# Performance work log

Hardware: AMD Instinct MI355X
Metric: run time of the kernel (lower is better)

The kernel has to match this reference:

```python
import jax, jax.numpy as jnp
import numpy as np
from jax import lax

B, T, H, E, V, S = 32, 512, 1024, 300, 32000, 50
NL2 = 4  # 2 layers * 2 directions of encoder hidden


def setup_inputs() -> dict:
    key = jax.random.key(0)
    ks = jax.random.split(key, 20)
    w = 0.05  # small init scale to keep tanh/softmax well-conditioned
    return {
        "enc_out": jax.random.normal(ks[0], (B, T, H), jnp.float32),
        "enc_h": jax.random.normal(ks[1], (NL2, B, H // 2), jnp.float32),
        "enc_c": jax.random.normal(ks[2], (NL2, B, H // 2), jnp.float32),
        "embedding": jax.random.normal(ks[3], (V, E), jnp.float32),
        "attn_W": jax.random.normal(ks[4], (H, 2 * H), jnp.float32) * w,
        "attn_b": jnp.zeros((H,), jnp.float32),
        "v": jax.random.normal(ks[5], (H,), jnp.float32) * w,
        "Wih0": jax.random.normal(ks[6], (4 * H, E + H), jnp.float32) * w,
        "Whh0": jax.random.normal(ks[7], (4 * H, H), jnp.float32) * w,
        "bih0": jnp.zeros((4 * H,), jnp.float32),
        "bhh0": jnp.zeros((4 * H,), jnp.float32),
        "Wih1": jax.random.normal(ks[8], (4 * H, H), jnp.float32) * w,
        "Whh1": jax.random.normal(ks[9], (4 * H, H), jnp.float32) * w,
        "bih1": jnp.zeros((4 * H,), jnp.float32),
        "bhh1": jnp.zeros((4 * H,), jnp.float32),
        "genW": jax.random.normal(ks[10], (V, H), jnp.float32) * w,
        "genb": jnp.zeros((V,), jnp.float32),
        "question": jax.random.randint(ks[11], (B, S), 0, V, jnp.int64),
    }


def _lstm_cell(x, h, c, Wih, Whh, bih, bhh):
    # torch gate order: i, f, g, o
    g = x @ Wih.T + bih + h @ Whh.T + bhh
    i, f, gg, o = jnp.split(g, 4, axis=-1)
    c2 = jax.nn.sigmoid(f) * c + jax.nn.sigmoid(i) * jnp.tanh(gg)
    h2 = jax.nn.sigmoid(o) * jnp.tanh(c2)
    return h2, c2


def reference(enc_out, enc_h, enc_c, embedding, attn_W, attn_b, v,
              Wih0, Whh0, bih0, bhh0, Wih1, Whh1, bih1, bhh1,
              genW, genb, question):
    # merge bidirectional encoder halves: (2L,B,H/2) -> (L,B,H)
    h0 = jnp.concatenate([enc_h[0::2], enc_h[1::2]], axis=2)
    c0 = jnp.concatenate([enc_c[0::2], enc_c[1::2]], axis=2)

    def step(carry, tok):
        h, c = carry  # each (L, B, H)
        emb = embedding[tok]  # (B, E); dropout is identity (eval mode)
        hid = h[-1]  # (B, H), last-layer hidden drives attention
        Hrep = jnp.broadcast_to(hid[:, None, :], enc_out.shape)  # (B,T,H)
        energy = jnp.tanh(jnp.concatenate([Hrep, enc_out], axis=-1) @ attn_W.T + attn_b)
        scores = jnp.einsum('bth,h->bt', energy, v)
        aw = jax.nn.softmax(scores, axis=1)  # (B, T)
        ctx = jnp.einsum('bt,bth->bh', aw, enc_out)  # (B, H)
        x = jnp.concatenate([emb, ctx], axis=-1)  # (B, E+H)
        h0n, c0n = _lstm_cell(x, h[0], c[0], Wih0, Whh0, bih0, bhh0)
        h1n, c1n = _lstm_cell(h0n, h[1], c[1], Wih1, Whh1, bih1, bhh1)
        out = jax.nn.log_softmax(h1n @ genW.T + genb, axis=-1)  # (B, V)
        return (jnp.stack([h0n, h1n]), jnp.stack([c0n, c1n])), out

    _, outs = lax.scan(step, (h0, c0), question.T)  # outs: (S, B, V)
    return jnp.transpose(outs, (1, 0, 2))  # (B, S, V)
```

## Files before the change

### kernel.cpp

```cpp
#include <hip/hip_runtime.h>
#include <hip/hip_bf16.h>
#include <math.h>

#define DEVI static __device__ __forceinline__

namespace {
constexpr int B = 32, T = 512, H = 1024, E = 300, V = 32000, S = 50;
constexpr int KX = E + H;
constexpr int K0 = 2368;
constexpr int K1 = 2048;
constexpr int MG = V + H;
}

typedef __bf16 bf16x8 __attribute__((ext_vector_type(8)));
typedef float f32x4 __attribute__((ext_vector_type(4)));

DEVI float bf2f(unsigned short u) { union { unsigned int i; float f; } v; v.i = (unsigned int)u << 16; return v.f; }
DEVI unsigned short f2bf(float f) {
  union { float f; unsigned int i; } v; v.f = f;
  unsigned int x = v.i;
  return (unsigned short)((x + 0x7fffu + ((x >> 16) & 1u)) >> 16);
}
#if __has_builtin(__builtin_amdgcn_rcpf)
DEVI float frcp(float x) { return __builtin_amdgcn_rcpf(x); }
#else
DEVI float frcp(float x) { return 1.0f / x; }
#endif
DEVI float sigm(float x) { return frcp(1.0f + __expf(-x)); }
DEVI float tanh_(float x) { return 1.0f - 2.0f * frcp(__expf(2.0f * x) + 1.0f); }

__global__ __launch_bounds__(256) void k_cast_gen(const float* __restrict__ genW,
    const float* __restrict__ attn_W, unsigned short* __restrict__ Wbig) {
  size_t i4 = ((size_t)blockIdx.x * 256 + threadIdx.x) * 4;
  if (i4 >= (size_t)MG * H) return;
  int row = (int)(i4 >> 10), k = (int)(i4 & 1023);
  const float* src = row < V ? &genW[((size_t)row << 10) + k]
                             : &attn_W[(size_t)(row - V) * (2 * H) + k];
  float4 v = *(const float4*)src;
  ushort4 o; o.x = f2bf(v.x); o.y = f2bf(v.y); o.z = f2bf(v.z); o.w = f2bf(v.w);
  *(ushort4*)&Wbig[i4] = o;
}

__global__ __launch_bounds__(256) void k_cast_l0(const float* __restrict__ Wih,
    const float* __restrict__ Whh, unsigned short* __restrict__ Wc) {
  int m = blockIdx.x;
  int g = m & 3, n = m >> 2, srow = g * H + n;
  for (int i = threadIdx.x; i < K0 / 4; i += 256) {
    int k = i * 4;
    float4 v;
    if (k < KX) v = *(const float4*)&Wih[(size_t)srow * KX + k];
    else if (k < KX + H) v = *(const float4*)&Whh[(size_t)srow * H + (k - KX)];
    else v = make_float4(0.f, 0.f, 0.f, 0.f);
    ushort4 o; o.x = f2bf(v.x); o.y = f2bf(v.y); o.z = f2bf(v.z); o.w = f2bf(v.w);
    *(ushort4*)&Wc[(size_t)m * K0 + k] = o;
  }
}

__global__ __launch_bounds__(256) void k_cast_l1(const float* __restrict__ Wih,
    const float* __restrict__ Whh, unsigned short* __restrict__ Wc) {
  int m = blockIdx.x;
  int g = m & 3, n = m >> 2, srow = g * H + n;
  for (int i = threadIdx.x; i < K1 / 4; i += 256) {
    int k = i * 4;
    float4 v = (k < H) ? *(const float4*)&Wih[(size_t)srow * H + k]
                       : *(const float4*)&Whh[(size_t)srow * H + (k - H)];
    ushort4 o; o.x = f2bf(v.x); o.y = f2bf(v.y); o.z = f2bf(v.z); o.w = f2bf(v.w);
    *(ushort4*)&Wc[(size_t)m * K1 + k] = o;
  }
}

__global__ __launch_bounds__(256) void k_cast_attnr(const float* __restrict__ attn_W,
                                                    unsigned short* __restrict__ Wr) {
  size_t i4 = ((size_t)blockIdx.x * 256 + threadIdx.x) * 4;
  if (i4 >= (size_t)H * H) return;
  int n = (int)(i4 >> 10), k = (int)(i4 & 1023);
  float4 v = *(const float4*)&attn_W[(size_t)n * (2 * H) + H + k];
  ushort4 o; o.x = f2bf(v.x); o.y = f2bf(v.y); o.z = f2bf(v.z); o.w = f2bf(v.w);
  *(ushort4*)&Wr[i4] = o;
}

__global__ void k_bias(const float* bih0, const float* bhh0,
                       const float* bih1, const float* bhh1,
                       float* bc0, float* bc1) {
  int idx = blockIdx.x * 256 + threadIdx.x;
  if (idx < 4096) { int g = idx & 3, n = idx >> 2; bc0[idx] = bih0[g * H + n] + bhh0[g * H + n]; }
  else if (idx < 8192) { int m = idx - 4096; int g = m & 3, n = m >> 2; bc1[m] = bih1[g * H + n] + bhh1[g * H + n]; }
}

__global__ __launch_bounds__(256) void k_cast_enc(const float* __restrict__ src,
                                                  unsigned short* __restrict__ dst) {
  size_t i4 = ((size_t)blockIdx.x * 256 + threadIdx.x) * 4;
  if (i4 >= (size_t)B * T * H) return;
  float4 v = *(const float4*)&src[i4];
  ushort4 o; o.x = f2bf(v.x); o.y = f2bf(v.y); o.z = f2bf(v.z); o.w = f2bf(v.w);
  *(ushort4*)&dst[i4] = o;
}

__global__ __launch_bounds__(256) void k_init(const float* __restrict__ enc_h,
    const float* __restrict__ enc_c, float* __restrict__ cbuf,
    unsigned short* __restrict__ xc0_0, unsigned short* __restrict__ xc0_1,
    unsigned short* __restrict__ xc1_0, unsigned short* __restrict__ hgen) {
  int idx = blockIdx.x * 256 + threadIdx.x;
  if (idx < 2 * B * H) {
    int l = idx >> 15, r = idx & 32767, b = r >> 10, hh = r & 1023;
    int half = hh >> 9, hr = hh & 511;
    int src = (2 * l + half) * B * (H / 2) + b * (H / 2) + hr;
    cbuf[idx] = enc_c[src];
    unsigned short hb = f2bf(enc_h[src]);
    if (l == 0) xc0_0[(size_t)b * K0 + KX + hh] = hb;
    else { xc1_0[(size_t)b * K1 + H + hh] = hb; hgen[(size_t)b * H + hh] = hb; }
  } else if (idx < 2 * B * H + 2 * B * 20) {
    int j = idx - 2 * B * H;
    int p = j / (B * 20), rr = j % (B * 20), b = rr / 20, kk = rr % 20;
    (p ? xc0_1 : xc0_0)[(size_t)b * K0 + KX + H + kk] = 0;
  }
}

__global__ __launch_bounds__(256) void k_encproj_mfma(const unsigned short* __restrict__ Wr,
    const unsigned short* __restrict__ Xb, const float* __restrict__ attn_b,
    unsigned short* __restrict__ encp) {
  int wv = threadIdx.x >> 6, lane = threadIdx.x & 63;
  int n0w = blockIdx.x * 64 + wv * 16;
  int m0 = blockIdx.y * 64;
  const unsigned short* Wp = Wr + (size_t)(n0w + (lane & 15)) * H + (lane >> 4) * 8;
  const unsigned short* Xp = Xb + (size_t)(m0 + (lane & 15)) * H + (lane >> 4) * 8;
  f32x4 acc[4] = {{0.f,0.f,0.f,0.f},{0.f,0.f,0.f,0.f},{0.f,0.f,0.f,0.f},{0.f,0.f,0.f,0.f}};
#pragma unroll 2
  for (int k0 = 0; k0 < H; k0 += 32) {
    bf16x8 a = *(const bf16x8*)(Wp + k0);
#pragma unroll
    for (int g = 0; g < 4; g++) {
      bf16x8 b = *(const bf16x8*)(Xp + (size_t)g * 16 * H + k0);
      acc[g] = __builtin_amdgcn_mfma_f32_16x16x32_bf16(a, b, acc[g], 0, 0, 0);
    }
  }
  int nb = n0w + (lane >> 4) * 4;
  f32x4 bi = *(const f32x4*)&attn_b[nb];
#pragma unroll
  for (int g = 0; g < 4; g++) {
    int m = m0 + g * 16 + (lane & 15);
    f32x4 o = acc[g] + bi;
    ushort4 ob; ob.x = f2bf(o[0]); ob.y = f2bf(o[1]); ob.z = f2bf(o[2]); ob.w = f2bf(o[3]);
    *(ushort4*)&encp[(size_t)m * H + nb] = ob;
  }
}

template <int K>
DEVI void gemm_tile(const unsigned short* __restrict__ W, const unsigned short* __restrict__ X,
                    int m0w, int lane, f32x4& acc0, f32x4& acc1) {
  const unsigned short* Wp = W + (size_t)(m0w + (lane & 15)) * K + (lane >> 4) * 8;
  const unsigned short* Xp = X + (size_t)(lane & 15) * K + (lane >> 4) * 8;
#pragma unroll 4
  for (int k0 = 0; k0 < K; k0 += 32) {
    bf16x8 a  = *(const bf16x8*)(Wp + k0);
    bf16x8 b0 = *(const bf16x8*)(Xp + k0);
    bf16x8 b1 = *(const bf16x8*)(Xp + 16 * K + k0);
    acc0 = __builtin_amdgcn_mfma_f32_16x16x32_bf16(a, b0, acc0, 0, 0, 0);
    acc1 = __builtin_amdgcn_mfma_f32_16x16x32_bf16(a, b1, acc1, 0, 0, 0);
  }
}

template <int K>
__global__ __launch_bounds__(256) void k_gemm_out(const unsigned short* __restrict__ W,
    const unsigned short* __restrict__ X, const float* __restrict__ bias, int M0,
    float* __restrict__ out0, int ld0, float* __restrict__ out1, int ld1,
    float* __restrict__ part) {
  __shared__ float esum[4][32];
  int wv = threadIdx.x >> 6, lane = threadIdx.x & 63;
  int m0w = blockIdx.x * 64 + wv * 16;
  f32x4 acc0 = {0.f, 0.f, 0.f, 0.f}, acc1 = acc0;
  gemm_tile<K>(W, X, m0w, lane, acc0, acc1);
  int r0 = m0w + (lane >> 4) * 4;
  int b = lane & 15;
  float s0 = 0.f, s1 = 0.f;
  if (r0 < M0) {
    f32x4 bi = *(const f32x4*)&bias[r0];
    f32x4 o0 = acc0 + bi, o1 = acc1 + bi;
    *(f32x4*)&out0[(size_t)b * ld0 + r0] = o0;
    *(f32x4*)&out0[(size_t)(b + 16) * ld0 + r0] = o1;
    s0 = __expf(o0[0]) + __expf(o0[1]) + __expf(o0[2]) + __expf(o0[3]);
    s1 = __expf(o1[0]) + __expf(o1[1]) + __expf(o1[2]) + __expf(o1[3]);
  } else {
    int r = r0 - M0;
    *(f32x4*)&out1[(size_t)b * ld1 + r] = acc0;
    *(f32x4*)&out1[(size_t)(b + 16) * ld1 + r] = acc1;
  }
  if (part != nullptr && blockIdx.x < V / 64) {
    s0 += __shfl_xor(s0, 16, 64); s0 += __shfl_xor(s0, 32, 64);
    s1 += __shfl_xor(s1, 16, 64); s1 += __shfl_xor(s1, 32, 64);
    if (lane < 16) { esum[wv][lane] = s0; esum[wv][lane + 16] = s1; }
    __syncthreads();
    if (threadIdx.x < 32)
      part[blockIdx.x * 32 + threadIdx.x] =
          esum[0][threadIdx.x] + esum[1][threadIdx.x] + esum[2][threadIdx.x] + esum[3][threadIdx.x];
  }
}

template <int K>
__global__ __launch_bounds__(256) void k_gemm_lstm(const unsigned short* __restrict__ W,
    const unsigned short* __restrict__ X, const float* __restrict__ bcomb,
    float* __restrict__ c,
    unsigned short* __restrict__ hA, int ldA_, int offA,
    unsigned short* __restrict__ hB, int ldB_, int offB) {
  __shared__ f32x4 red[4][64][2];
  int wv = threadIdx.x >> 6, lane = threadIdx.x & 63;
  int m0w = blockIdx.x * 16;
  const unsigned short* Wp = W + (size_t)(m0w + (lane & 15)) * K + (lane >> 4) * 8;
  const unsigned short* Xp = X + (size_t)(lane & 15) * K + (lane >> 4) * 8;
  f32x4 acc0 = {0.f, 0.f, 0.f, 0.f}, acc1 = acc0;
#pragma unroll 2
  for (int k0 = wv * 32; k0 < K; k0 += 128) {
    bf16x8 a  = *(const bf16x8*)(Wp + k0);
    bf16x8 b0 = *(const bf16x8*)(Xp + k0);
    bf16x8 b1 = *(const bf16x8*)(Xp + 16 * K + k0);
    acc0 = __builtin_amdgcn_mfma_f32_16x16x32_bf16(a, b0, acc0, 0, 0, 0);
    acc1 = __builtin_amdgcn_mfma_f32_16x16x32_bf16(a, b1, acc1, 0, 0, 0);
  }
  red[wv][lane][0] = acc0;
  red[wv][lane][1] = acc1;
  __syncthreads();
  if (wv == 0) {
    acc0 = red[0][lane][0] + red[1][lane][0] + red[2][lane][0] + red[3][lane][0];
    acc1 = red[0][lane][1] + red[1][lane][1] + red[2][lane][1] + red[3][lane][1];
    int r0 = m0w + (lane >> 4) * 4;
    int n = r0 >> 2;
    f32x4 bi = *(const f32x4*)&bcomb[r0];
#pragma unroll
    for (int f = 0; f < 2; f++) {
      f32x4 g = f ? acc1 : acc0;
      int b = (lane & 15) + f * 16;
      float gi = g[0] + bi[0], gf = g[1] + bi[1];
      float gg = g[2] + bi[2], go = g[3] + bi[3];
      float cp = c[(size_t)b * H + n];
      float c2 = sigm(gf) * cp + sigm(gi) * tanh_(gg);
      c[(size_t)b * H + n] = c2;
      unsigned short hb = f2bf(sigm(go) * tanh_(c2));
      hA[(size_t)b * ldA_ + offA + n] = hb;
      hB[(size_t)b * ldB_ + offB + n] = hb;
    }
  }
}

__global__ __launch_bounds__(256) void k_p1(const unsigned short* __restrict__ encp,
    const float* __restrict__ hidproj, const float* __restrict__ vvec,
    float* __restrict__ scores,
    const float* __restrict__ logits, const float* __restrict__ part,
    float* __restrict__ out,
    const float* __restrict__ embedding, const int* __restrict__ question,
    unsigned short* __restrict__ xc, int s) {
  int bx = blockIdx.x, tid = threadIdx.x;
  if (bx < 4096) {
    int wid = bx * 4 + (tid >> 6);
    int lane = tid & 63;
    int b = wid >> 9;
    const unsigned short* ep = encp + (size_t)wid * H;
    const float* hp = hidproj + (size_t)b * H;
    float acc = 0.f;
#pragma unroll
    for (int i = 0; i < 2; i++) {
      int base = i * 512 + lane * 8;
      uint4 u = *(const uint4*)&ep[base];
      float4 h0 = *(const float4*)&hp[base];
      float4 h1 = *(const float4*)&hp[base + 4];
      float4 v0 = *(const float4*)&vvec[base];
      float4 v1 = *(const float4*)&vvec[base + 4];
      acc += v0.x * tanh_(bf2f((unsigned short)(u.x & 0xffff)) + h0.x);
      acc += v0.y * tanh_(bf2f((unsigned short)(u.x >> 16)) + h0.y);
      acc += v0.z * tanh_(bf2f((unsigned short)(u.y & 0xffff)) + h0.z);
      acc += v0.w * tanh_(bf2f((unsigned short)(u.y >> 16)) + h0.w);
      acc += v1.x * tanh_(bf2f((unsigned short)(u.z & 0xffff)) + h1.x);
      acc += v1.y * tanh_(bf2f((unsigned short)(u.z >> 16)) + h1.y);
      acc += v1.z * tanh_(bf2f((unsigned short)(u.w & 0xffff)) + h1.z);
      acc += v1.w * tanh_(bf2f((unsigned short)(u.w >> 16)) + h1.w);
    }
#pragma unroll
    for (int off = 32; off; off >>= 1) acc += __shfl_xor(acc, off, 64);
    if (lane == 0) scores[wid] = acc;
  } else if (bx < 4352) {
    if (s == 0) return;
    __shared__ float red[256];
    int idx = bx - 4096;
    int b = idx >> 3, ch = idx & 7;
    float ssum = 0.f;
    for (int i = tid; i < V / 64; i += 256) ssum += part[i * 32 + b];
    red[tid] = ssum; __syncthreads();
    for (int st = 128; st; st >>= 1) { if (tid < st) red[tid] += red[tid + st]; __syncthreads(); }
    float lse = __logf(red[0]);
    const float* L = logits + (size_t)b * V + ch * 4000;
    float* O = out + ((size_t)b * S + (s - 1)) * V + ch * 4000;
    for (int i = tid; i < 1000; i += 256) {
      float4 v = ((const float4*)L)[i];
      ((float4*)O)[i] = make_float4(v.x - lse, v.y - lse, v.z - lse, v.w - lse);
    }
  } else {
    int b = bx - 4352;
    int tok = question[b * S + s];
    for (int e = tid; e < E; e += 256)
      xc[(size_t)b * K0 + e] = f2bf(embedding[(size_t)tok * E + e]);
  }
}

__global__ __launch_bounds__(256) void k_ctx(const float* __restrict__ scores,
    const unsigned short* __restrict__ enc_bf, unsigned short* __restrict__ xc) {
  int b = blockIdx.x, y = blockIdx.y, tid = threadIdx.x;
  __shared__ float aw[T];
  __shared__ float red[256];
  float s0 = scores[b * T + tid], s1 = scores[b * T + 256 + tid];
  float m = fmaxf(s0, s1);
  red[tid] = m; __syncthreads();
  for (int st = 128; st; st >>= 1) { if (tid < st) red[tid] = fmaxf(red[tid], red[tid + st]); __syncthreads(); }
  m = red[0]; __syncthreads();
  float e0 = __expf(s0 - m), e1 = __expf(s1 - m);
  aw[tid] = e0; aw[tid + 256] = e1;
  red[tid] = e0 + e1; __syncthreads();
  for (int st = 128; st; st >>= 1) { if (tid < st) red[tid] += red[tid + st]; __syncthreads(); }
  float inv = frcp(red[0]);
  __syncthreads();
  int wv = tid >> 6, l = tid & 63;
  int q = l & 15, tp = l >> 4;
  const unsigned short* eb = enc_bf + (size_t)b * T * H + y * 64 + q * 4;
  float a0 = 0.f, a1 = 0.f, a2 = 0.f, a3 = 0.f;
  for (int it = 0; it < 32; it++) {
    int t = it * 16 + wv * 4 + tp;
    uint2 u = *(const uint2*)&eb[(size_t)t * H];
    float w = aw[t];
    a0 += w * bf2f((unsigned short)(u.x & 0xffff));
    a1 += w * bf2f((unsigned short)(u.x >> 16));
    a2 += w * bf2f((unsigned short)(u.y & 0xffff));
    a3 += w * bf2f((unsigned short)(u.y >> 16));
  }
  a0 += __shfl_xor(a0, 16, 64); a0 += __shfl_xor(a0, 32, 64);
  a1 += __shfl_xor(a1, 16, 64); a1 += __shfl_xor(a1, 32, 64);
  a2 += __shfl_xor(a2, 16, 64); a2 += __shfl_xor(a2, 32, 64);
  a3 += __shfl_xor(a3, 16, 64); a3 += __shfl_xor(a3, 32, 64);
  __syncthreads();
  if (tp == 0) {
    red[wv * 64 + q * 4 + 0] = a0; red[wv * 64 + q * 4 + 1] = a1;
    red[wv * 64 + q * 4 + 2] = a2; red[wv * 64 + q * 4 + 3] = a3;
  }
  __syncthreads();
  if (tid < 64) {
    float val = (red[tid] + red[64 + tid] + red[128 + tid] + red[192 + tid]) * inv;
    xc[(size_t)b * K0 + E + y * 64 + tid] = f2bf(val);
  }
}

__global__ __launch_bounds__(256) void k_lsB(const float* __restrict__ logits,
    const float* __restrict__ part, float* __restrict__ out, int s) {
  int b = blockIdx.x, ch = blockIdx.y, tid = threadIdx.x;
  __shared__ float red[256];
  float ssum = 0.f;
  for (int i = tid; i < V / 64; i += 256) ssum += part[i * 32 + b];
  red[tid] = ssum; __syncthreads();
  for (int st = 128; st; st >>= 1) { if (tid < st) red[tid] += red[tid + st]; __syncthreads(); }
  float lse = __logf(red[0]);
  const float* L = logits + (size_t)b * V + ch * 4000;
  float* O = out + ((size_t)b * S + s) * V + ch * 4000;
  for (int i = tid; i < 1000; i += 256) {
    float4 v = ((const float4*)L)[i];
    ((float4*)O)[i] = make_float4(v.x - lse, v.y - lse, v.z - lse, v.w - lse);
  }
}

extern "C" void kernel_launch(void* const* d_in, const int* in_sizes, int n_in,
                              void* d_out, int out_size, void* d_ws, size_t ws_size,
                              hipStream_t stream) {
  const float* enc_out   = (const float*)d_in[0];
  const float* enc_h     = (const float*)d_in[1];
  const float* enc_c     = (const float*)d_in[2];
  const float* embedding = (const float*)d_in[3];
  const float* attn_W    = (const float*)d_in[4];
  const float* attn_b    = (const float*)d_in[5];
  const float* vvec      = (const float*)d_in[6];
  const float* Wih0      = (const float*)d_in[7];
  const float* Whh0      = (const float*)d_in[8];
  const float* bih0      = (const float*)d_in[9];
  const float* bhh0      = (const float*)d_in[10];
  const float* Wih1      = (const float*)d_in[11];
  const float* Whh1      = (const float*)d_in[12];
  const float* bih1      = (const float*)d_in[13];
  const float* bhh1      = (const float*)d_in[14];
  const float* genW      = (const float*)d_in[15];
  const float* genb      = (const float*)d_in[16];
  const int*   question  = (const int*)d_in[17];
  float* out = (float*)d_out;

  char* w = (char*)d_ws;
  auto alloc = [&](size_t bytes) { char* r = w; w += (bytes + 255) & ~(size_t)255; return r; };
  unsigned short* Wbig  = (unsigned short*)alloc((size_t)MG * H * 2);
  unsigned short* Wc0   = (unsigned short*)alloc((size_t)4096 * K0 * 2);
  unsigned short* Wc1   = (unsigned short*)alloc((size_t)4096 * K1 * 2);
  unsigned short* encb  = (unsigned short*)alloc((size_t)B * T * H * 2);
  unsigned short* encp  = (unsigned short*)alloc((size_t)B * T * H * 2);
  unsigned short* Wr    = (unsigned short*)alloc((size_t)H * H * 2);
  float* bcomb0 = (float*)alloc(4096 * 4);
  float* bcomb1 = (float*)alloc(4096 * 4);
  float* cbuf   = (float*)alloc((size_t)2 * B * H * 4);
  unsigned short* xc0[2] = {(unsigned short*)alloc((size_t)B * K0 * 2),
                            (unsigned short*)alloc((size_t)B * K0 * 2)};
  unsigned short* xc1[2] = {(unsigned short*)alloc((size_t)B * K1 * 2),
                            (unsigned short*)alloc((size_t)B * K1 * 2)};
  unsigned short* hgen  = (unsigned short*)alloc((size_t)B * H * 2);
  float* hidproj = (float*)alloc((size_t)B * H * 4);
  float* scores  = (float*)alloc((size_t)B * T * 4);
  float* logits  = (float*)alloc((size_t)B * V * 4);
  float* part    = (float*)alloc((size_t)(V / 64) * 32 * 4);

  k_cast_gen<<<(int)(((size_t)MG * H / 4 + 255) / 256), 256, 0, stream>>>(genW, attn_W, Wbig);
  k_cast_l0<<<4096, 256, 0, stream>>>(Wih0, Whh0, Wc0);
  k_cast_l1<<<4096, 256, 0, stream>>>(Wih1, Whh1, Wc1);
  k_cast_attnr<<<H * H / 4 / 256, 256, 0, stream>>>(attn_W, Wr);
  k_bias<<<32, 256, 0, stream>>>(bih0, bhh0, bih1, bhh1, bcomb0, bcomb1);
  k_cast_enc<<<(B * T * H / 4) / 256, 256, 0, stream>>>(enc_out, encb);
  k_init<<<(2 * B * H + 2 * B * 20 + 255) / 256, 256, 0, stream>>>(
      enc_h, enc_c, cbuf, xc0[0], xc0[1], xc1[0], hgen);
  k_encproj_mfma<<<dim3(H / 64, B * T / 64), 256, 0, stream>>>(Wr, encb, attn_b, encp);
  k_gemm_out<1024><<<H / 64, 256, 0, stream>>>(
      Wbig + (size_t)V * H, hgen, nullptr, 0, nullptr, 0, hidproj, H, nullptr);

  for (int s = 0; s < S; s++) {
    int par = s & 1;
    k_p1<<<4384, 256, 0, stream>>>(encp, hidproj, vvec, scores,
                                   logits, part, out, embedding, question, xc0[par], s);
    k_ctx<<<dim3(B, 16), 256, 0, stream>>>(scores, encb, xc0[par]);
    k_gemm_lstm<K0><<<4096 / 16, 256, 0, stream>>>(
        Wc0, xc0[par], bcomb0, cbuf,
        xc0[par ^ 1], K0, KX,
        xc1[par], K1, 0);
    k_gemm_lstm<K1><<<4096 / 16, 256, 0, stream>>>(
        Wc1, xc1[par], bcomb1, cbuf + B * H,
        xc1[par ^ 1], K1, H,
        hgen, H, 0);
    k_gemm_out<1024><<<MG / 64, 256, 0, stream>>>(
        Wbig, hgen, genb, V, logits, V, hidproj, H, part);
  }
  k_lsB<<<dim3(B, 8), 256, 0, stream>>>(logits, part, out, S - 1);
}
```

Baseline: 3.957 ms.

## Defer vocab projection GEMM into next step's attention kernel to shorten critical path

```diff
diff --git a/kernel.cpp b/kernel.cpp
--- a/kernel.cpp
+++ b/kernel.cpp
@@ -244,13 +244,37 @@
 __global__ __launch_bounds__(256) void k_p1(const unsigned short* __restrict__ encp,
     const float* __restrict__ hidproj, const float* __restrict__ vvec,
     float* __restrict__ scores,
-    const float* __restrict__ logits, const float* __restrict__ part,
+    const unsigned short* __restrict__ Wbig, const unsigned short* __restrict__ hgen,
+    const float* __restrict__ genb,
+    float* __restrict__ logitsW, float* __restrict__ partW,
+    const float* __restrict__ logitsR, const float* __restrict__ partR,
     float* __restrict__ out,
     const float* __restrict__ embedding, const int* __restrict__ question,
     unsigned short* __restrict__ xc, int s) {
   int bx = blockIdx.x, tid = threadIdx.x;
-  if (bx < 4096) {
-    int wid = bx * 4 + (tid >> 6);
+  if (bx < 500) {
+    if (s == 0) return;
+    __shared__ float esum[4][32];
+    int wv = tid >> 6, lane = tid & 63;
+    int m0w = bx * 64 + wv * 16;
+    f32x4 acc0 = {0.f, 0.f, 0.f, 0.f}, acc1 = acc0;
+    gemm_tile<1024>(Wbig, hgen, m0w, lane, acc0, acc1);
+    int r0 = m0w + (lane >> 4) * 4;
+    int b = lane & 15;
+    f32x4 bi = *(const f32x4*)&genb[r0];
+    f32x4 o0 = acc0 + bi, o1 = acc1 + bi;
+    *(f32x4*)&logitsW[(size_t)b * V + r0] = o0;
+    *(f32x4*)&logitsW[(size_t)(b + 16) * V + r0] = o1;
+    float s0 = __expf(o0[0]) + __expf(o0[1]) + __expf(o0[2]) + __expf(o0[3]);
+    float s1 = __expf(o1[0]) + __expf(o1[1]) + __expf(o1[2]) + __expf(o1[3]);
+    s0 += __shfl_xor(s0, 16, 64); s0 += __shfl_xor(s0, 32, 64);
+    s1 += __shfl_xor(s1, 16, 64); s1 += __shfl_xor(s1, 32, 64);
+    if (lane < 16) { esum[wv][lane] = s0; esum[wv][lane + 16] = s1; }
+    __syncthreads();
+    if (tid < 32)
+      partW[bx * 32 + tid] = esum[0][tid] + esum[1][tid] + esum[2][tid] + esum[3][tid];
+  } else if (bx < 4596) {
+    int wid = (bx - 500) * 4 + (tid >> 6);
     int lane = tid & 63;
     int b = wid >> 9;
     const unsigned short* ep = encp + (size_t)wid * H;
@@ -276,24 +300,24 @@
 #pragma unroll
     for (int off = 32; off; off >>= 1) acc += __shfl_xor(acc, off, 64);
     if (lane == 0) scores[wid] = acc;
-  } else if (bx < 4352) {
-    if (s == 0) return;
+  } else if (bx < 4852) {
+    if (s < 2) return;
     __shared__ float red[256];
-    int idx = bx - 4096;
+    int idx = bx - 4596;
     int b = idx >> 3, ch = idx & 7;
     float ssum = 0.f;
-    for (int i = tid; i < V / 64; i += 256) ssum += part[i * 32 + b];
+    for (int i = tid; i < V / 64; i += 256) ssum += partR[i * 32 + b];
     red[tid] = ssum; __syncthreads();
     for (int st = 128; st; st >>= 1) { if (tid < st) red[tid] += red[tid + st]; __syncthreads(); }
     float lse = __logf(red[0]);
-    const float* L = logits + (size_t)b * V + ch * 4000;
-    float* O = out + ((size_t)b * S + (s - 1)) * V + ch * 4000;
+    const float* L = logitsR + (size_t)b * V + ch * 4000;
+    float* O = out + ((size_t)b * S + (s - 2)) * V + ch * 4000;
     for (int i = tid; i < 1000; i += 256) {
       float4 v = ((const float4*)L)[i];
       ((float4*)O)[i] = make_float4(v.x - lse, v.y - lse, v.z - lse, v.w - lse);
     }
   } else {
-    int b = bx - 4352;
+    int b = bx - 4852;
     int tok = question[b * S + s];
     for (int e = tid; e < E; e += 256)
       xc[(size_t)b * K0 + e] = f2bf(embedding[(size_t)tok * E + e]);
@@ -403,8 +427,8 @@
   unsigned short* hgen  = (unsigned short*)alloc((size_t)B * H * 2);
   float* hidproj = (float*)alloc((size_t)B * H * 4);
   float* scores  = (float*)alloc((size_t)B * T * 4);
-  float* logits  = (float*)alloc((size_t)B * V * 4);
-  float* part    = (float*)alloc((size_t)(V / 64) * 32 * 4);
+  float* logits[2] = {(float*)alloc((size_t)B * V * 4), (float*)alloc((size_t)B * V * 4)};
+  float* part[2]   = {(float*)alloc((size_t)(V / 64) * 32 * 4), (float*)alloc((size_t)(V / 64) * 32 * 4)};
 
   k_cast_gen<<<(int)(((size_t)MG * H / 4 + 255) / 256), 256, 0, stream>>>(genW, attn_W, Wbig);
   k_cast_l0<<<4096, 256, 0, stream>>>(Wih0, Whh0, Wc0);
@@ -420,8 +444,11 @@
 
   for (int s = 0; s < S; s++) {
     int par = s & 1;
-    k_p1<<<4384, 256, 0, stream>>>(encp, hidproj, vvec, scores,
-                                   logits, part, out, embedding, question, xc0[par], s);
+    k_p1<<<4884, 256, 0, stream>>>(encp, hidproj, vvec, scores,
+                                   Wbig, hgen, genb,
+                                   logits[par ^ 1], part[par ^ 1],
+                                   logits[par], part[par],
+                                   out, embedding, question, xc0[par], s);
     k_ctx<<<dim3(B, 16), 256, 0, stream>>>(scores, encb, xc0[par]);
     k_gemm_lstm<K0><<<4096 / 16, 256, 0, stream>>>(
         Wc0, xc0[par], bcomb0, cbuf,
@@ -431,8 +458,11 @@
         Wc1, xc1[par], bcomb1, cbuf + B * H,
         xc1[par ^ 1], K1, H,
         hgen, H, 0);
-    k_gemm_out<1024><<<MG / 64, 256, 0, stream>>>(
-        Wbig, hgen, genb, V, logits, V, hidproj, H, part);
-  }
-  k_lsB<<<dim3(B, 8), 256, 0, stream>>>(logits, part, out, S - 1);
-}
+    k_gemm_out<1024><<<H / 64, 256, 0, stream>>>(
+        Wbig + (size_t)V * H, hgen, nullptr, 0, nullptr, 0, hidproj, H, nullptr);
+  }
+  k_gemm_out<1024><<<V / 64, 256, 0, stream>>>(
+      Wbig, hgen, genb, V, logits[(S - 1) & 1], V, hidproj, H, part[(S - 1) & 1]);
+  k_lsB<<<dim3(B, 8), 256, 0, stream>>>(logits[(S - 2) & 1], part[(S - 2) & 1], out, S - 2);
+  k_lsB<<<dim3(B, 8), 256, 0, stream>>>(logits[(S - 1) & 1], part[(S - 1) & 1], out, S - 1);
+}
```

Result: slower. 4.037 ms (+2.0%).

## Quantize generator and attention-hidden weights to FP8 and rebatch score kernel

Applied to the files above, without the earlier changes.

```diff
diff --git a/kernel.cpp b/kernel.cpp
--- a/kernel.cpp
+++ b/kernel.cpp
@@ -20,6 +20,23 @@
   union { float f; unsigned int i; } v; v.f = f;
   unsigned int x = v.i;
   return (unsigned short)((x + 0x7fffu + ((x >> 16) & 1u)) >> 16);
+}
+DEVI unsigned char f2e4m3(float x) {
+  union { float f; unsigned int u; } v;
+  v.f = x;
+  unsigned int s = (v.u >> 24) & 0x80u;
+  v.u &= 0x7FFFFFFFu;
+  if (v.f >= 448.0f) return (unsigned char)(s | 0x7E);
+  if (v.f < 0.015625f) {
+    int q = (int)rintf(v.f * 512.0f);
+    return (unsigned char)(s | (unsigned int)q);
+  }
+  unsigned int u = v.u;
+  unsigned int lsb = (u >> 20) & 1u;
+  u += 0x0007FFFFu + lsb;
+  unsigned int exp = (u >> 23) - 120u;
+  unsigned int man = (u >> 20) & 7u;
+  return (unsigned char)(s | (exp << 3) | man);
 }
 #if __has_builtin(__builtin_amdgcn_rcpf)
 DEVI float frcp(float x) { return __builtin_amdgcn_rcpf(x); }
@@ -30,15 +47,15 @@
 DEVI float tanh_(float x) { return 1.0f - 2.0f * frcp(__expf(2.0f * x) + 1.0f); }
 
 __global__ __launch_bounds__(256) void k_cast_gen(const float* __restrict__ genW,
-    const float* __restrict__ attn_W, unsigned short* __restrict__ Wbig) {
+    const float* __restrict__ attn_W, unsigned char* __restrict__ Wbig8) {
   size_t i4 = ((size_t)blockIdx.x * 256 + threadIdx.x) * 4;
   if (i4 >= (size_t)MG * H) return;
   int row = (int)(i4 >> 10), k = (int)(i4 & 1023);
   const float* src = row < V ? &genW[((size_t)row << 10) + k]
                              : &attn_W[(size_t)(row - V) * (2 * H) + k];
   float4 v = *(const float4*)src;
-  ushort4 o; o.x = f2bf(v.x); o.y = f2bf(v.y); o.z = f2bf(v.z); o.w = f2bf(v.w);
-  *(ushort4*)&Wbig[i4] = o;
+  uchar4 o; o.x = f2e4m3(v.x); o.y = f2e4m3(v.y); o.z = f2e4m3(v.z); o.w = f2e4m3(v.w);
+  *(uchar4*)&Wbig8[i4] = o;
 }
 
 __global__ __launch_bounds__(256) void k_cast_l0(const float* __restrict__ Wih,
@@ -99,16 +116,16 @@
 __global__ __launch_bounds__(256) void k_init(const float* __restrict__ enc_h,
     const float* __restrict__ enc_c, float* __restrict__ cbuf,
     unsigned short* __restrict__ xc0_0, unsigned short* __restrict__ xc0_1,
-    unsigned short* __restrict__ xc1_0, unsigned short* __restrict__ hgen) {
+    unsigned short* __restrict__ xc1_0, unsigned char* __restrict__ hgen8) {
   int idx = blockIdx.x * 256 + threadIdx.x;
   if (idx < 2 * B * H) {
     int l = idx >> 15, r = idx & 32767, b = r >> 10, hh = r & 1023;
     int half = hh >> 9, hr = hh & 511;
     int src = (2 * l + half) * B * (H / 2) + b * (H / 2) + hr;
     cbuf[idx] = enc_c[src];
-    unsigned short hb = f2bf(enc_h[src]);
-    if (l == 0) xc0_0[(size_t)b * K0 + KX + hh] = hb;
-    else { xc1_0[(size_t)b * K1 + H + hh] = hb; hgen[(size_t)b * H + hh] = hb; }
+    float hv = enc_h[src];
+    if (l == 0) xc0_0[(size_t)b * K0 + KX + hh] = f2bf(hv);
+    else { xc1_0[(size_t)b * K1 + H + hh] = f2bf(hv); hgen8[(size_t)b * H + hh] = f2e4m3(hv); }
   } else if (idx < 2 * B * H + 2 * B * 20) {
     int j = idx - 2 * B * H;
     int p = j / (B * 20), rr = j % (B * 20), b = rr / 20, kk = rr % 20;
@@ -145,31 +162,29 @@
   }
 }
 
-template <int K>
-DEVI void gemm_tile(const unsigned short* __restrict__ W, const unsigned short* __restrict__ X,
-                    int m0w, int lane, f32x4& acc0, f32x4& acc1) {
-  const unsigned short* Wp = W + (size_t)(m0w + (lane & 15)) * K + (lane >> 4) * 8;
-  const unsigned short* Xp = X + (size_t)(lane & 15) * K + (lane >> 4) * 8;
+DEVI void gemm_tile_fp8(const unsigned char* __restrict__ W, const unsigned char* __restrict__ X,
+                        int m0w, int lane, f32x4& acc0, f32x4& acc1) {
+  const unsigned char* Wp = W + (size_t)(m0w + (lane & 15)) * 1024 + (lane >> 4) * 8;
+  const unsigned char* Xp = X + (size_t)(lane & 15) * 1024 + (lane >> 4) * 8;
 #pragma unroll 4
-  for (int k0 = 0; k0 < K; k0 += 32) {
-    bf16x8 a  = *(const bf16x8*)(Wp + k0);
-    bf16x8 b0 = *(const bf16x8*)(Xp + k0);
-    bf16x8 b1 = *(const bf16x8*)(Xp + 16 * K + k0);
-    acc0 = __builtin_amdgcn_mfma_f32_16x16x32_bf16(a, b0, acc0, 0, 0, 0);
-    acc1 = __builtin_amdgcn_mfma_f32_16x16x32_bf16(a, b1, acc1, 0, 0, 0);
-  }
-}
-
-template <int K>
-__global__ __launch_bounds__(256) void k_gemm_out(const unsigned short* __restrict__ W,
-    const unsigned short* __restrict__ X, const float* __restrict__ bias, int M0,
+  for (int k0 = 0; k0 < 1024; k0 += 32) {
+    long a  = *(const long*)(Wp + k0);
+    long b0 = *(const long*)(Xp + k0);
+    long b1 = *(const long*)(Xp + 16 * 1024 + k0);
+    acc0 = __builtin_amdgcn_mfma_f32_16x16x32_fp8_fp8(a, b0, acc0, 0, 0, 0);
+    acc1 = __builtin_amdgcn_mfma_f32_16x16x32_fp8_fp8(a, b1, acc1, 0, 0, 0);
+  }
+}
+
+__global__ __launch_bounds__(256) void k_gemm_out_fp8(const unsigned char* __restrict__ W,
+    const unsigned char* __restrict__ X, const float* __restrict__ bias, int M0,
     float* __restrict__ out0, int ld0, float* __restrict__ out1, int ld1,
     float* __restrict__ part) {
   __shared__ float esum[4][32];
   int wv = threadIdx.x >> 6, lane = threadIdx.x & 63;
   int m0w = blockIdx.x * 64 + wv * 16;
   f32x4 acc0 = {0.f, 0.f, 0.f, 0.f}, acc1 = acc0;
-  gemm_tile<K>(W, X, m0w, lane, acc0, acc1);
+  gemm_tile_fp8(W, X, m0w, lane, acc0, acc1);
   int r0 = m0w + (lane >> 4) * 4;
   int b = lane & 15;
   float s0 = 0.f, s1 = 0.f;
@@ -201,7 +216,8 @@
     const unsigned short* __restrict__ X, const float* __restrict__ bcomb,
     float* __restrict__ c,
     unsigned short* __restrict__ hA, int ldA_, int offA,
-    unsigned short* __restrict__ hB, int ldB_, int offB) {
+    unsigned short* __restrict__ hB, int ldB_, int offB,
+    unsigned char* __restrict__ h8) {
   __shared__ f32x4 red[4][64][2];
   int wv = threadIdx.x >> 6, lane = threadIdx.x & 63;
   int m0w = blockIdx.x * 16;
@@ -234,9 +250,11 @@
       float cp = c[(size_t)b * H + n];
       float c2 = sigm(gf) * cp + sigm(gi) * tanh_(gg);
       c[(size_t)b * H + n] = c2;
-      unsigned short hb = f2bf(sigm(go) * tanh_(c2));
+      float h2 = sigm(go) * tanh_(c2);
+      unsigned short hb = f2bf(h2);
       hA[(size_t)b * ldA_ + offA + n] = hb;
       hB[(size_t)b * ldB_ + offB + n] = hb;
+      if (h8) h8[(size_t)b * H + n] = f2e4m3(h2);
     }
   }
 }
@@ -249,37 +267,45 @@
     const float* __restrict__ embedding, const int* __restrict__ question,
     unsigned short* __restrict__ xc, int s) {
   int bx = blockIdx.x, tid = threadIdx.x;
-  if (bx < 4096) {
-    int wid = bx * 4 + (tid >> 6);
-    int lane = tid & 63;
-    int b = wid >> 9;
-    const unsigned short* ep = encp + (size_t)wid * H;
+  if (bx < 1024) {
+    int wv = tid >> 6, lane = tid & 63;
+    int wid0 = bx * 16 + wv * 4;
+    int b = wid0 >> 9;
     const float* hp = hidproj + (size_t)b * H;
-    float acc = 0.f;
+    float4 h0a[2], h1a[2], v0a[2], v1a[2];
 #pragma unroll
     for (int i = 0; i < 2; i++) {
       int base = i * 512 + lane * 8;
-      uint4 u = *(const uint4*)&ep[base];
-      float4 h0 = *(const float4*)&hp[base];
-      float4 h1 = *(const float4*)&hp[base + 4];
-      float4 v0 = *(const float4*)&vvec[base];
-      float4 v1 = *(const float4*)&vvec[base + 4];
-      acc += v0.x * tanh_(bf2f((unsigned short)(u.x & 0xffff)) + h0.x);
-      acc += v0.y * tanh_(bf2f((unsigned short)(u.x >> 16)) + h0.y);
-      acc += v0.z * tanh_(bf2f((unsigned short)(u.y & 0xffff)) + h0.z);
-      acc += v0.w * tanh_(bf2f((unsigned short)(u.y >> 16)) + h0.w);
-      acc += v1.x * tanh_(bf2f((unsigned short)(u.z & 0xffff)) + h1.x);
-      acc += v1.y * tanh_(bf2f((unsigned short)(u.z >> 16)) + h1.y);
-      acc += v1.z * tanh_(bf2f((unsigned short)(u.w & 0xffff)) + h1.z);
-      acc += v1.w * tanh_(bf2f((unsigned short)(u.w >> 16)) + h1.w);
+      h0a[i] = *(const float4*)&hp[base];
+      h1a[i] = *(const float4*)&hp[base + 4];
+      v0a[i] = *(const float4*)&vvec[base];
+      v1a[i] = *(const float4*)&vvec[base + 4];
     }
 #pragma unroll
-    for (int off = 32; off; off >>= 1) acc += __shfl_xor(acc, off, 64);
-    if (lane == 0) scores[wid] = acc;
-  } else if (bx < 4352) {
+    for (int j = 0; j < 4; j++) {
+      const unsigned short* ep = encp + (size_t)(wid0 + j) * H;
+      float acc = 0.f;
+#pragma unroll
+      for (int i = 0; i < 2; i++) {
+        int base = i * 512 + lane * 8;
+        uint4 u = *(const uint4*)&ep[base];
+        acc += v0a[i].x * tanh_(bf2f((unsigned short)(u.x & 0xffff)) + h0a[i].x);
+        acc += v0a[i].y * tanh_(bf2f((unsigned short)(u.x >> 16)) + h0a[i].y);
+        acc += v0a[i].z * tanh_(bf2f((unsigned short)(u.y & 0xffff)) + h0a[i].z);
+        acc += v0a[i].w * tanh_(bf2f((unsigned short)(u.y >> 16)) + h0a[i].w);
+        acc += v1a[i].x * tanh_(bf2f((unsigned short)(u.z & 0xffff)) + h1a[i].x);
+        acc += v1a[i].y * tanh_(bf2f((unsigned short)(u.z >> 16)) + h1a[i].y);
+        acc += v1a[i].z * tanh_(bf2f((unsigned short)(u.w & 0xffff)) + h1a[i].z);
+        acc += v1a[i].w * tanh_(bf2f((unsigned short)(u.w >> 16)) + h1a[i].w);
+      }
+#pragma unroll
+      for (int off = 32; off; off >>= 1) acc += __shfl_xor(acc, off, 64);
+      if (lane == 0) scores[wid0 + j] = acc;
+    }
+  } else if (bx < 1280) {
     if (s == 0) return;
     __shared__ float red[256];
-    int idx = bx - 4096;
+    int idx = bx - 1024;
     int b = idx >> 3, ch = idx & 7;
     float ssum = 0.f;
     for (int i = tid; i < V / 64; i += 256) ssum += part[i * 32 + b];
@@ -293,7 +319,7 @@
       ((float4*)O)[i] = make_float4(v.x - lse, v.y - lse, v.z - lse, v.w - lse);
     }
   } else {
-    int b = bx - 4352;
+    int b = bx - 1280;
     int tok = question[b * S + s];
     for (int e = tid; e < E; e += 256)
       xc[(size_t)b * K0 + e] = f2bf(embedding[(size_t)tok * E + e]);
@@ -387,7 +413,7 @@
 
   char* w = (char*)d_ws;
   auto alloc = [&](size_t bytes) { char* r = w; w += (bytes + 255) & ~(size_t)255; return r; };
-  unsigned short* Wbig  = (unsigned short*)alloc((size_t)MG * H * 2);
+  unsigned char*  Wbig8 = (unsigned char*)alloc((size_t)MG * H);
   unsigned short* Wc0   = (unsigned short*)alloc((size_t)4096 * K0 * 2);
   unsigned short* Wc1   = (unsigned short*)alloc((size_t)4096 * K1 * 2);
   unsigned short* encb  = (unsigned short*)alloc((size_t)B * T * H * 2);
@@ -401,38 +427,41 @@
   unsigned short* xc1[2] = {(unsigned short*)alloc((size_t)B * K1 * 2),
                             (unsigned short*)alloc((size_t)B * K1 * 2)};
   unsigned short* hgen  = (unsigned short*)alloc((size_t)B * H * 2);
+  unsigned char*  hgen8 = (unsigned char*)alloc((size_t)B * H);
   float* hidproj = (float*)alloc((size_t)B * H * 4);
   float* scores  = (float*)alloc((size_t)B * T * 4);
   float* logits  = (float*)alloc((size_t)B * V * 4);
   float* part    = (float*)alloc((size_t)(V / 64) * 32 * 4);
 
-  k_cast_gen<<<(int)(((size_t)MG * H / 4 + 255) / 256), 256, 0, stream>>>(genW, attn_W, Wbig);
+  k_cast_gen<<<(int)(((size_t)MG * H / 4 + 255) / 256), 256, 0, stream>>>(genW, attn_W, Wbig8);
   k_cast_l0<<<4096, 256, 0, stream>>>(Wih0, Whh0, Wc0);
   k_cast_l1<<<4096, 256, 0, stream>>>(Wih1, Whh1, Wc1);
   k_cast_attnr<<<H * H / 4 / 256, 256, 0, stream>>>(attn_W, Wr);
   k_bias<<<32, 256, 0, stream>>>(bih0, bhh0, bih1, bhh1, bcomb0, bcomb1);
   k_cast_enc<<<(B * T * H / 4) / 256, 256, 0, stream>>>(enc_out, encb);
   k_init<<<(2 * B * H + 2 * B * 20 + 255) / 256, 256, 0, stream>>>(
-      enc_h, enc_c, cbuf, xc0[0], xc0[1], xc1[0], hgen);
+      enc_h, enc_c, cbuf, xc0[0], xc0[1], xc1[0], hgen8);
   k_encproj_mfma<<<dim3(H / 64, B * T / 64), 256, 0, stream>>>(Wr, encb, attn_b, encp);
-  k_gemm_out<1024><<<H / 64, 256, 0, stream>>>(
-      Wbig + (size_t)V * H, hgen, nullptr, 0, nullptr, 0, hidproj, H, nullptr);
+  k_gemm_out_fp8<<<H / 64, 256, 0, stream>>>(
+      Wbig8 + (size_t)V * H, hgen8, nullptr, 0, nullptr, 0, hidproj, H, nullptr);
 
   for (int s = 0; s < S; s++) {
     int par = s & 1;
-    k_p1<<<4384, 256, 0, stream>>>(encp, hidproj, vvec, scores,
+    k_p1<<<1312, 256, 0, stream>>>(encp, hidproj, vvec, scores,
                                    logits, part, out, embedding, question, xc0[par], s);
     k_ctx<<<dim3(B, 16), 256, 0, stream>>>(scores, encb, xc0[par]);
     k_gemm_lstm<K0><<<4096 / 16, 256, 0, stream>>>(
         Wc0, xc0[par], bcomb0, cbuf,
         xc0[par ^ 1], K0, KX,
-        xc1[par], K1, 0);
+        xc1[par], K1, 0,
+        nullptr);
     k_gemm_lstm<K1><<<4096 / 16, 256, 0, stream>>>(
         Wc1, xc1[par], bcomb1, cbuf + B * H,
         xc1[par ^ 1], K1, H,
-        hgen, H, 0);
-    k_gemm_out<1024><<<MG / 64, 256, 0, stream>>>(
-        Wbig, hgen, genb, V, logits, V, hidproj, H, part);
+        hgen, H, 0,
+        hgen8);
+    k_gemm_out_fp8<<<MG / 64, 256, 0, stream>>>(
+        Wbig8, hgen8, genb, V, logits, V, hidproj, H, part);
   }
   k_lsB<<<dim3(B, 8), 256, 0, stream>>>(logits, part, out, S - 1);
 }
```

Measured after the change: 3.955 ms. About the same (-0.0%).
